# Kernel optimization log

Hardware: AMD Instinct MI355X
Metric: run time of the kernel (lower is better)

The kernel has to match this reference:

```python
import jax, jax.numpy as jnp
import numpy as np

N = 4096
NFEAT = 512
NHID = 60
NCLASS = 4


def setup_inputs() -> dict:
    key = jax.random.key(0)
    ks = jax.random.split(key, 12)
    x = jax.random.normal(ks[0], (N, NFEAT), dtype=jnp.float32)
    # sparse-ish binary adjacency (sub_adj), symmetric not required by the module
    sub_adj = (jax.random.uniform(ks[1], (N, N)) < 0.002).astype(jnp.float32)
    # P_vec: init to ones (torch.sub in reset_parameters is non-inplace, so it stays ones)
    P_vec = jnp.ones((N * (N + 1) // 2,), dtype=jnp.float32)
    s1 = 1.0 / np.sqrt(NFEAT)
    s2 = 1.0 / np.sqrt(NHID)
    W1 = jax.random.normal(ks[2], (NFEAT, NHID), dtype=jnp.float32) * s1
    b1 = jax.random.normal(ks[3], (NHID,), dtype=jnp.float32) * 0.01
    W2 = jax.random.normal(ks[4], (NHID, NHID), dtype=jnp.float32) * s2
    b2 = jax.random.normal(ks[5], (NHID,), dtype=jnp.float32) * 0.01
    W3 = jax.random.normal(ks[6], (NHID, NHID), dtype=jnp.float32) * s2
    b3 = jax.random.normal(ks[7], (NHID,), dtype=jnp.float32) * 0.01
    lin_w = jax.random.normal(ks[8], (NHID, NCLASS), dtype=jnp.float32) * s2
    lin_b = jax.random.normal(ks[9], (NCLASS,), dtype=jnp.float32) * 0.01
    return {"x": x, "sub_adj": sub_adj, "P_vec": P_vec,
            "W1": W1, "b1": b1, "W2": W2, "b2": b2, "W3": W3, "b3": b3,
            "lin_w": lin_w, "lin_b": lin_b}


def reference(x, sub_adj, P_vec, W1, b1, W2, b2, W3, b3, lin_w, lin_b):
    n = sub_adj.shape[0]
    # scatter P_vec into lower triangle (incl. diagonal), then symmetrize
    il, jl = jnp.tril_indices(n)
    M = jnp.zeros((n, n), dtype=P_vec.dtype).at[il, jl].set(P_vec)
    P_hat_symm = M + M.T - jnp.diag(jnp.diag(M))
    # perturbed adjacency with self-loops
    A_tilde = jax.nn.sigmoid(P_hat_symm) * sub_adj + jnp.eye(n, dtype=P_vec.dtype)
    # degree (column sums, matching python sum(adj)); detached in the original
    d = jax.lax.stop_gradient(jnp.sum(A_tilde, axis=0))
    d_inv_sqrt = jnp.where(d > 0, d ** -0.5, 0.0)  # isinf -> 0
    # D^{-1/2} A D^{-1/2} without materializing diag matrices
    norm_adj = d_inv_sqrt[:, None] * A_tilde * d_inv_sqrt[None, :]
    # 3 GCN layers: spmm(norm_adj, x @ W) + b
    h1 = jax.nn.relu(norm_adj @ (x @ W1) + b1)
    h2 = jax.nn.relu(norm_adj @ (h1 @ W2) + b2)
    h3 = norm_adj @ (h2 @ W3) + b3
    logits = h3 @ lin_w + lin_b  # dropout is identity in eval / p=0
    return jax.nn.log_softmax(logits, axis=1)
```

## Files before the change

kernel.cpp:

```cpp
#include <hip/hip_runtime.h>
#include <math.h>

#define NN 4096
#define NFEAT 512
#define NHID 60
#define NCLASS 4
#define CAP 96
#define GSTRIDE 64

__global__ __launch_bounds__(256) void k_scan(const float* __restrict__ adj,
                                              const float* __restrict__ P,
                                              float* __restrict__ dcol,
                                              int* __restrict__ cnt,
                                              int* __restrict__ cols,
                                              float* __restrict__ vals) {
    const int v = blockIdx.x * 256 + threadIdx.x;
    const float4 a = ((const float4*)adj)[v];
    if (a.x + a.y + a.z + a.w == 0.f) return;
    const float av[4] = {a.x, a.y, a.z, a.w};
    const int e0 = v * 4;
    #pragma unroll
    for (int q = 0; q < 4; ++q) {
        if (av[q] != 0.f) {
            const int e = e0 + q;
            const int i = e >> 12;
            const int j = e & (NN - 1);
            const int hi = i > j ? i : j;
            const int lo = i > j ? j : i;
            const float pv = P[((hi * (hi + 1)) >> 1) + lo];
            const float s = av[q] / (1.f + __expf(-pv));
            atomicAdd(&dcol[j], s);
            const int pos = atomicAdd(&cnt[i], 1);
            if (pos < CAP) { cols[i * CAP + pos] = j; vals[i * CAP + pos] = s; }
        }
    }
}

__global__ __launch_bounds__(256) void k_xw(const float* __restrict__ x,
                                            const float* __restrict__ W1,
                                            float* __restrict__ g1) {
    __shared__ float part[1024];
    const int tid = threadIdx.x;
    const int w = tid >> 6, lane = tid & 63;
    const int c = lane < NHID ? lane : 0;
    const int row0 = blockIdx.x * 4;
    const int k0 = w * (NFEAT / 4);
    const float* x0 = x + (row0 + 0) * NFEAT;
    const float* x1 = x + (row0 + 1) * NFEAT;
    const float* x2 = x + (row0 + 2) * NFEAT;
    const float* x3 = x + (row0 + 3) * NFEAT;
    float a0 = 0.f, a1 = 0.f, a2 = 0.f, a3 = 0.f;
    for (int k = k0; k < k0 + NFEAT / 4; k += 4) {
        const float4 xv0 = *(const float4*)(x0 + k);
        const float4 xv1 = *(const float4*)(x1 + k);
        const float4 xv2 = *(const float4*)(x2 + k);
        const float4 xv3 = *(const float4*)(x3 + k);
        const float w0 = W1[(k + 0) * NHID + c];
        const float w1 = W1[(k + 1) * NHID + c];
        const float w2 = W1[(k + 2) * NHID + c];
        const float w3 = W1[(k + 3) * NHID + c];
        a0 = fmaf(xv0.x, w0, fmaf(xv0.y, w1, fmaf(xv0.z, w2, fmaf(xv0.w, w3, a0))));
        a1 = fmaf(xv1.x, w0, fmaf(xv1.y, w1, fmaf(xv1.z, w2, fmaf(xv1.w, w3, a1))));
        a2 = fmaf(xv2.x, w0, fmaf(xv2.y, w1, fmaf(xv2.z, w2, fmaf(xv2.w, w3, a2))));
        a3 = fmaf(xv3.x, w0, fmaf(xv3.y, w1, fmaf(xv3.z, w2, fmaf(xv3.w, w3, a3))));
    }
    part[(w * 4 + 0) * 64 + lane] = a0;
    part[(w * 4 + 1) * 64 + lane] = a1;
    part[(w * 4 + 2) * 64 + lane] = a2;
    part[(w * 4 + 3) * 64 + lane] = a3;
    __syncthreads();
    const float o = part[(0 * 4 + w) * 64 + lane] + part[(1 * 4 + w) * 64 + lane]
                  + part[(2 * 4 + w) * 64 + lane] + part[(3 * 4 + w) * 64 + lane];
    g1[(row0 + w) * GSTRIDE + lane] = (lane < NHID) ? o : 0.f;
}

__device__ __forceinline__ float spmm_row(const float* __restrict__ gin,
                                          const float* __restrict__ dcol,
                                          const int* __restrict__ cnt,
                                          const int* __restrict__ cols,
                                          const float* __restrict__ vals,
                                          int i, int lane, float di) {
    const int nn = min(cnt[i], CAP);
    float acc = gin[i * GSTRIDE + lane] * di;
    const int4*   c4 = (const int4*)(cols + i * CAP);
    const float4* v4 = (const float4*)(vals + i * CAP);
    int e = 0;
    for (; e + 4 <= nn; e += 4) {
        const int4   jj = c4[e >> 2];
        const float4 vv = v4[e >> 2];
        const float f0 = vv.x * rsqrtf(1.f + dcol[jj.x]);
        const float f1 = vv.y * rsqrtf(1.f + dcol[jj.y]);
        const float f2 = vv.z * rsqrtf(1.f + dcol[jj.z]);
        const float f3 = vv.w * rsqrtf(1.f + dcol[jj.w]);
        const float g0 = gin[jj.x * GSTRIDE + lane];
        const float g1 = gin[jj.y * GSTRIDE + lane];
        const float g2 = gin[jj.z * GSTRIDE + lane];
        const float g3 = gin[jj.w * GSTRIDE + lane];
        acc = fmaf(f0, g0, fmaf(f1, g1, fmaf(f2, g2, fmaf(f3, g3, acc))));
    }
    for (; e < nn; ++e) {
        const int j = cols[i * CAP + e];
        const float f = vals[i * CAP + e] * rsqrtf(1.f + dcol[j]);
        acc = fmaf(f, gin[j * GSTRIDE + lane], acc);
    }
    return acc * di;
}

__global__ __launch_bounds__(64) void k_layer(const float* __restrict__ gin,
                                              float* __restrict__ gout,
                                              const float* __restrict__ dcol,
                                              const int* __restrict__ cnt,
                                              const int* __restrict__ cols,
                                              const float* __restrict__ vals,
                                              const float* __restrict__ bias,
                                              const float* __restrict__ W) {
    __shared__ float hs[64];
    const int i = blockIdx.x;
    const int lane = threadIdx.x;
    const float di = rsqrtf(1.f + dcol[i]);
    const float acc = spmm_row(gin, dcol, cnt, cols, vals, i, lane, di);
    float hv = 0.f;
    if (lane < NHID) hv = fmaxf(acc + bias[lane], 0.f);
    hs[lane] = hv;
    __syncthreads();
    const int c = lane < NHID ? lane : 0;
    float o = 0.f;
    #pragma unroll 4
    for (int k = 0; k < NHID; ++k)
        o = fmaf(hs[k], W[k * NHID + c], o);
    gout[i * GSTRIDE + lane] = (lane < NHID) ? o : 0.f;
}

__global__ __launch_bounds__(64) void k_final(const float* __restrict__ gin,
                                              float* __restrict__ out,
                                              const float* __restrict__ dcol,
                                              const int* __restrict__ cnt,
                                              const int* __restrict__ cols,
                                              const float* __restrict__ vals,
                                              const float* __restrict__ b3,
                                              const float* __restrict__ lw,
                                              const float* __restrict__ lb) {
    __shared__ float hs[64];
    const int i = blockIdx.x;
    const int lane = threadIdx.x;
    const float di = rsqrtf(1.f + dcol[i]);
    const float acc = spmm_row(gin, dcol, cnt, cols, vals, i, lane, di);
    hs[lane] = (lane < NHID) ? acc + b3[lane] : 0.f;
    __syncthreads();
    if (lane < NCLASS) {
        float o = lb[lane];
        #pragma unroll 4
        for (int k = 0; k < NHID; ++k)
            o = fmaf(hs[k], lw[k * NCLASS + lane], o);
        float m = fmaxf(o, __shfl_xor(o, 1));
        m = fmaxf(m, __shfl_xor(m, 2));
        const float ex = __expf(o - m);
        float ss = ex + __shfl_xor(ex, 1);
        ss += __shfl_xor(ss, 2);
        out[i * NCLASS + lane] = o - m - __logf(ss);
    }
}

extern "C" void kernel_launch(void* const* d_in, const int* in_sizes, int n_in,
                              void* d_out, int out_size, void* d_ws, size_t ws_size,
                              hipStream_t stream) {
    const float* x   = (const float*)d_in[0];
    const float* adj = (const float*)d_in[1];
    const float* P   = (const float*)d_in[2];
    const float* W1  = (const float*)d_in[3];
    const float* b1  = (const float*)d_in[4];
    const float* W2  = (const float*)d_in[5];
    const float* b2  = (const float*)d_in[6];
    const float* W3  = (const float*)d_in[7];
    const float* b3  = (const float*)d_in[8];
    const float* lw  = (const float*)d_in[9];
    const float* lb  = (const float*)d_in[10];
    float* out = (float*)d_out;

    char* ws = (char*)d_ws;
    float* dcol = (float*)(ws);
    int*   cnt  = (int*)(ws + 16384);
    int*   cols = (int*)(ws + 32768);
    float* vals = (float*)(ws + 32768 + 1572864);
    float* bufA = (float*)(ws + 32768 + 2 * 1572864);
    float* bufB = (float*)(ws + 32768 + 2 * 1572864 + 1048576);

    hipMemsetAsync(ws, 0, 32768, stream);

    k_scan <<<(NN * NN / 4) / 256, 256, 0, stream>>>(adj, P, dcol, cnt, cols, vals);
    k_xw   <<<NN / 4, 256, 0, stream>>>(x, W1, bufA);
    k_layer<<<NN, 64, 0, stream>>>(bufA, bufB, dcol, cnt, cols, vals, b1, W2);
    k_layer<<<NN, 64, 0, stream>>>(bufB, bufA, dcol, cnt, cols, vals, b2, W3);
    k_final<<<NN, 64, 0, stream>>>(bufA, out, dcol, cnt, cols, vals, b3, lw, lb);
}
```

Baseline: 191.3 us.

## Fuse all GCN stages into one cooperative persistent kernel with grid syncs

Replaces the memset and five separate launches with one cooperative kernel of 1024 blocks. It zeroes the counters in-kernel, overlaps the x@W1 product with a grid-strided adjacency scan, and separates the three sparse layers with grid.sync barriers. Each block handles four rows per layer instead of one. This removes per-launch overhead and gaps between launches, at the cost of grid-wide barriers and the residency limit on cooperative launches. If the cooperative launch fails, the original multi-kernel path runs instead.

New measurement: 601.6 us. 214% more time.

```diff
diff --git a/kernel.cpp b/kernel.cpp
--- a/kernel.cpp
+++ b/kernel.cpp
@@ -1,5 +1,8 @@
 #include <hip/hip_runtime.h>
+#include <hip/hip_cooperative_groups.h>
 #include <math.h>
+
+namespace cg = cooperative_groups;
 
 #define NN 4096
 #define NFEAT 512
@@ -7,6 +10,186 @@
 #define NCLASS 4
 #define CAP 96
 #define GSTRIDE 64
+#define NBLK 1024
+#define NTHR 256
+#define SCAN_IT ((NN * NN / 4) / (NBLK * NTHR))
+
+__device__ __forceinline__ float spmm_row(const float* __restrict__ gin,
+                                          const float* __restrict__ dcol,
+                                          const int* __restrict__ cnt,
+                                          const int* __restrict__ cols,
+                                          const float* __restrict__ vals,
+                                          int i, int lane, float di) {
+    const int nn = min(cnt[i], CAP);
+    float acc = gin[i * GSTRIDE + lane] * di;
+    const int4*   c4 = (const int4*)(cols + i * CAP);
+    const float4* v4 = (const float4*)(vals + i * CAP);
+    int e = 0;
+    for (; e + 4 <= nn; e += 4) {
+        const int4   jj = c4[e >> 2];
+        const float4 vv = v4[e >> 2];
+        const float f0 = vv.x * rsqrtf(1.f + dcol[jj.x]);
+        const float f1 = vv.y * rsqrtf(1.f + dcol[jj.y]);
+        const float f2 = vv.z * rsqrtf(1.f + dcol[jj.z]);
+        const float f3 = vv.w * rsqrtf(1.f + dcol[jj.w]);
+        const float g0 = gin[jj.x * GSTRIDE + lane];
+        const float g1 = gin[jj.y * GSTRIDE + lane];
+        const float g2 = gin[jj.z * GSTRIDE + lane];
+        const float g3 = gin[jj.w * GSTRIDE + lane];
+        acc = fmaf(f0, g0, fmaf(f1, g1, fmaf(f2, g2, fmaf(f3, g3, acc))));
+    }
+    for (; e < nn; ++e) {
+        const int j = cols[i * CAP + e];
+        const float f = vals[i * CAP + e] * rsqrtf(1.f + dcol[j]);
+        acc = fmaf(f, gin[j * GSTRIDE + lane], acc);
+    }
+    return acc * di;
+}
+
+
+__device__ __forceinline__ void layer_phase(const float* __restrict__ gin,
+                                            float* __restrict__ gout,
+                                            const float* __restrict__ dcol,
+                                            const int* __restrict__ cnt,
+                                            const int* __restrict__ cols,
+                                            const float* __restrict__ vals,
+                                            const float* __restrict__ bias,
+                                            const float* __restrict__ W,
+                                            float* __restrict__ smem) {
+    const int w = threadIdx.x >> 6, lane = threadIdx.x & 63;
+    const int i = blockIdx.x * 4 + w;
+    const float di = rsqrtf(1.f + dcol[i]);
+    const float acc = spmm_row(gin, dcol, cnt, cols, vals, i, lane, di);
+    float hv = 0.f;
+    if (lane < NHID) hv = fmaxf(acc + bias[lane], 0.f);
+    float* hs = smem + w * 64;
+    hs[lane] = hv;
+    __syncthreads();
+    const int c = lane < NHID ? lane : 0;
+    float o = 0.f;
+    #pragma unroll 4
+    for (int k = 0; k < NHID; ++k)
+        o = fmaf(hs[k], W[k * NHID + c], o);
+    gout[i * GSTRIDE + lane] = (lane < NHID) ? o : 0.f;
+}
+
+__device__ __forceinline__ void final_phase(const float* __restrict__ gin,
+                                            float* __restrict__ out,
+                                            const float* __restrict__ dcol,
+                                            const int* __restrict__ cnt,
+                                            const int* __restrict__ cols,
+                                            const float* __restrict__ vals,
+                                            const float* __restrict__ b3,
+                                            const float* __restrict__ lw,
+                                            const float* __restrict__ lb,
+                                            float* __restrict__ smem) {
+    const int w = threadIdx.x >> 6, lane = threadIdx.x & 63;
+    const int i = blockIdx.x * 4 + w;
+    const float di = rsqrtf(1.f + dcol[i]);
+    const float acc = spmm_row(gin, dcol, cnt, cols, vals, i, lane, di);
+    float* hs = smem + w * 64;
+    hs[lane] = (lane < NHID) ? acc + b3[lane] : 0.f;
+    __syncthreads();
+    if (lane < NCLASS) {
+        float o = lb[lane];
+        #pragma unroll 4
+        for (int k = 0; k < NHID; ++k)
+            o = fmaf(hs[k], lw[k * NCLASS + lane], o);
+        float m = fmaxf(o, __shfl_xor(o, 1));
+        m = fmaxf(m, __shfl_xor(m, 2));
+        const float ex = __expf(o - m);
+        float ss = ex + __shfl_xor(ex, 1);
+        ss += __shfl_xor(ss, 2);
+        out[i * NCLASS + lane] = o - m - __logf(ss);
+    }
+}
+
+__global__ __launch_bounds__(NTHR, 4) void k_fused(
+    const float* __restrict__ x,  const float* __restrict__ adj,
+    const float* __restrict__ P,  const float* __restrict__ W1,
+    const float* __restrict__ b1, const float* __restrict__ W2,
+    const float* __restrict__ b2, const float* __restrict__ W3,
+    const float* __restrict__ b3, const float* __restrict__ lw,
+    const float* __restrict__ lb, float* __restrict__ out,
+    float* __restrict__ dcol, int* __restrict__ cnt,
+    int* __restrict__ cols,   float* __restrict__ vals,
+    float* __restrict__ bufA, float* __restrict__ bufB) {
+    cg::grid_group grid = cg::this_grid();
+    __shared__ float smem[1024];
+    const int tid = threadIdx.x;
+    const int t = blockIdx.x * NTHR + tid;
+
+    if (t < NN) { dcol[t] = 0.f; cnt[t] = 0; }
+    grid.sync();
+
+    {
+        const int w = tid >> 6, lane = tid & 63;
+        const int c = lane < NHID ? lane : 0;
+        const int row0 = blockIdx.x * 4;
+        const int k0 = w * (NFEAT / 4);
+        const float* x0 = x + (row0 + 0) * NFEAT;
+        const float* x1 = x + (row0 + 1) * NFEAT;
+        const float* x2 = x + (row0 + 2) * NFEAT;
+        const float* x3 = x + (row0 + 3) * NFEAT;
+        float a0 = 0.f, a1 = 0.f, a2 = 0.f, a3 = 0.f;
+        for (int k = k0; k < k0 + NFEAT / 4; k += 4) {
+            const float4 xv0 = *(const float4*)(x0 + k);
+            const float4 xv1 = *(const float4*)(x1 + k);
+            const float4 xv2 = *(const float4*)(x2 + k);
+            const float4 xv3 = *(const float4*)(x3 + k);
+            const float w0 = W1[(k + 0) * NHID + c];
+            const float w1 = W1[(k + 1) * NHID + c];
+            const float w2 = W1[(k + 2) * NHID + c];
+            const float w3 = W1[(k + 3) * NHID + c];
+            a0 = fmaf(xv0.x, w0, fmaf(xv0.y, w1, fmaf(xv0.z, w2, fmaf(xv0.w, w3, a0))));
+            a1 = fmaf(xv1.x, w0, fmaf(xv1.y, w1, fmaf(xv1.z, w2, fmaf(xv1.w, w3, a1))));
+            a2 = fmaf(xv2.x, w0, fmaf(xv2.y, w1, fmaf(xv2.z, w2, fmaf(xv2.w, w3, a2))));
+            a3 = fmaf(xv3.x, w0, fmaf(xv3.y, w1, fmaf(xv3.z, w2, fmaf(xv3.w, w3, a3))));
+        }
+        smem[(w * 4 + 0) * 64 + lane] = a0;
+        smem[(w * 4 + 1) * 64 + lane] = a1;
+        smem[(w * 4 + 2) * 64 + lane] = a2;
+        smem[(w * 4 + 3) * 64 + lane] = a3;
+        __syncthreads();
+        const float o = smem[(0 * 4 + w) * 64 + lane] + smem[(1 * 4 + w) * 64 + lane]
+                      + smem[(2 * 4 + w) * 64 + lane] + smem[(3 * 4 + w) * 64 + lane];
+        bufA[(row0 + w) * GSTRIDE + lane] = (lane < NHID) ? o : 0.f;
+    }
+
+    {
+        #pragma unroll 4
+        for (int it = 0; it < SCAN_IT; ++it) {
+            const int v = t + it * (NBLK * NTHR);
+            const float4 a = ((const float4*)adj)[v];
+            if (a.x + a.y + a.z + a.w == 0.f) continue;
+            const float av[4] = {a.x, a.y, a.z, a.w};
+            const int e0 = v * 4;
+            #pragma unroll
+            for (int q = 0; q < 4; ++q) {
+                if (av[q] != 0.f) {
+                    const int e = e0 + q;
+                    const int i = e >> 12;
+                    const int j = e & (NN - 1);
+                    const int hi = i > j ? i : j;
+                    const int lo = i > j ? j : i;
+                    const float pv = P[((hi * (hi + 1)) >> 1) + lo];
+                    const float s = av[q] / (1.f + __expf(-pv));
+                    atomicAdd(&dcol[j], s);
+                    const int pos = atomicAdd(&cnt[i], 1);
+                    if (pos < CAP) { cols[i * CAP + pos] = j; vals[i * CAP + pos] = s; }
+                }
+            }
+        }
+    }
+    grid.sync();
+
+    layer_phase(bufA, bufB, dcol, cnt, cols, vals, b1, W2, smem);
+    grid.sync();
+    layer_phase(bufB, bufA, dcol, cnt, cols, vals, b2, W3, smem);
+    grid.sync();
+    final_phase(bufA, out, dcol, cnt, cols, vals, b3, lw, lb, smem);
+}
+
 
 __global__ __launch_bounds__(256) void k_scan(const float* __restrict__ adj,
                                               const float* __restrict__ P,
@@ -74,38 +257,6 @@
     g1[(row0 + w) * GSTRIDE + lane] = (lane < NHID) ? o : 0.f;
 }
 
-__device__ __forceinline__ float spmm_row(const float* __restrict__ gin,
-                                          const float* __restrict__ dcol,
-                                          const int* __restrict__ cnt,
-                                          const int* __restrict__ cols,
-                                          const float* __restrict__ vals,
-                                          int i, int lane, float di) {
-    const int nn = min(cnt[i], CAP);
-    float acc = gin[i * GSTRIDE + lane] * di;
-    const int4*   c4 = (const int4*)(cols + i * CAP);
-    const float4* v4 = (const float4*)(vals + i * CAP);
-    int e = 0;
-    for (; e + 4 <= nn; e += 4) {
-        const int4   jj = c4[e >> 2];
-        const float4 vv = v4[e >> 2];
-        const float f0 = vv.x * rsqrtf(1.f + dcol[jj.x]);
-        const float f1 = vv.y * rsqrtf(1.f + dcol[jj.y]);
-        const float f2 = vv.z * rsqrtf(1.f + dcol[jj.z]);
-        const float f3 = vv.w * rsqrtf(1.f + dcol[jj.w]);
-        const float g0 = gin[jj.x * GSTRIDE + lane];
-        const float g1 = gin[jj.y * GSTRIDE + lane];
-        const float g2 = gin[jj.z * GSTRIDE + lane];
-        const float g3 = gin[jj.w * GSTRIDE + lane];
-        acc = fmaf(f0, g0, fmaf(f1, g1, fmaf(f2, g2, fmaf(f3, g3, acc))));
-    }
-    for (; e < nn; ++e) {
-        const int j = cols[i * CAP + e];
-        const float f = vals[i * CAP + e] * rsqrtf(1.f + dcol[j]);
-        acc = fmaf(f, gin[j * GSTRIDE + lane], acc);
-    }
-    return acc * di;
-}
-
 __global__ __launch_bounds__(64) void k_layer(const float* __restrict__ gin,
                                               float* __restrict__ gout,
                                               const float* __restrict__ dcol,
@@ -185,11 +336,20 @@
     float* bufA = (float*)(ws + 32768 + 2 * 1572864);
     float* bufB = (float*)(ws + 32768 + 2 * 1572864 + 1048576);
 
-    hipMemsetAsync(ws, 0, 32768, stream);
-
-    k_scan <<<(NN * NN / 4) / 256, 256, 0, stream>>>(adj, P, dcol, cnt, cols, vals);
-    k_xw   <<<NN / 4, 256, 0, stream>>>(x, W1, bufA);
-    k_layer<<<NN, 64, 0, stream>>>(bufA, bufB, dcol, cnt, cols, vals, b1, W2);
-    k_layer<<<NN, 64, 0, stream>>>(bufB, bufA, dcol, cnt, cols, vals, b2, W3);
-    k_final<<<NN, 64, 0, stream>>>(bufA, out, dcol, cnt, cols, vals, b3, lw, lb);
-}
+    void* kp[] = { (void*)&x,  (void*)&adj, (void*)&P,  (void*)&W1, (void*)&b1,
+                   (void*)&W2, (void*)&b2,  (void*)&W3, (void*)&b3, (void*)&lw,
+                   (void*)&lb, (void*)&out, (void*)&dcol, (void*)&cnt,
+                   (void*)&cols, (void*)&vals, (void*)&bufA, (void*)&bufB };
+
+    hipError_t e = hipLaunchCooperativeKernel((const void*)k_fused,
+                                              dim3(NBLK), dim3(NTHR),
+                                              kp, 0, stream);
+    if (e != hipSuccess) {
+        hipMemsetAsync(ws, 0, 32768, stream);
+        k_scan <<<(NN * NN / 4) / 256, 256, 0, stream>>>(adj, P, dcol, cnt, cols, vals);
+        k_xw   <<<NN / 4, 256, 0, stream>>>(x, W1, bufA);
+        k_layer<<<NN, 64, 0, stream>>>(bufA, bufB, dcol, cnt, cols, vals, b1, W2);
+        k_layer<<<NN, 64, 0, stream>>>(bufB, bufA, dcol, cnt, cols, vals, b2, W3);
+        k_final<<<NN, 64, 0, stream>>>(bufA, out, dcol, cnt, cols, vals, b3, lw, lb);
+    }
+}
```
